# Performance work log

Measured on AMD Instinct MI355X. Metric: run time of the kernel, lower is better.

Reference implementation:

```python
import jax, jax.numpy as jnp
import numpy as np

# Mamba2 config fixed by the wrapper: state=32, expand=1, n_groups=1, conv kernel=4
H, P, N, K = 32, 64, 32, 4          # heads, head_dim, state_size, conv kernel
D_MODEL = H * P                      # hidden = intermediate (expand=1) = 2048
CONV_DIM = D_MODEL + 2 * N           # intermediate + 2*n_groups*state = 2112
PROJ = D_MODEL + CONV_DIM + H        # in_proj width = 4192
EPS = 1e-6


def setup_inputs() -> dict:
    key = jax.random.key(0)
    ks = jax.random.split(key, 8)
    B, L = 4, 2048
    w = lambda k, shape, sc=0.02: jax.random.normal(k, shape, jnp.float32) * sc
    return {
        "x": jax.random.normal(ks[0], (B, L, D_MODEL), jnp.float32),
        "W_in": w(ks[1], (D_MODEL, PROJ)),
        "b_in": jnp.zeros((PROJ,), jnp.float32),
        "conv_w": w(ks[2], (CONV_DIM, K), 0.25),
        "conv_b": jnp.zeros((CONV_DIM,), jnp.float32),
        "A_log": jnp.log(jnp.arange(1, H + 1, dtype=jnp.float32)),
        "dt_bias": jax.random.uniform(ks[3], (H,), jnp.float32, -4.0, 0.0),
        "D_param": jnp.ones((H,), jnp.float32),
        "norm_w": jnp.ones((D_MODEL,), jnp.float32),
        "W_out": w(ks[4], (D_MODEL, D_MODEL)),
    }


def reference(x, W_in, b_in, conv_w, conv_b, A_log, dt_bias, D_param, norm_w, W_out):
    B, L, _ = x.shape
    proj = x @ W_in + b_in                                   # (B,L,PROJ)
    gate, hBC, dt_raw = jnp.split(proj, [D_MODEL, D_MODEL + CONV_DIM], axis=-1)

    # causal depthwise conv1d over time (kernel K, left pad K-1), then SiLU
    hp = jnp.pad(hBC, ((0, 0), (K - 1, 0), (0, 0)))
    conv = conv_b + sum(hp[:, k:k + L, :] * conv_w[:, k] for k in range(K))
    conv = jax.nn.silu(conv)

    xs, Bm, Cm = jnp.split(conv, [D_MODEL, D_MODEL + N], axis=-1)
    xs = xs.reshape(B, L, H, P)                              # (B,L,H,P)

    A = -jnp.exp(A_log)                                      # (H,)
    dt = jax.nn.softplus(dt_raw + dt_bias)                   # (B,L,H)
    dA = jnp.exp(dt * A)                                     # (B,L,H)

    def step(hstate, inp):
        dA_t, dt_t, x_t, B_t, C_t = inp                      # (B,H),(B,H),(B,H,P),(B,N),(B,N)
        upd = (dt_t[:, :, None] * x_t)[..., None] * B_t[:, None, None, :]
        hstate = dA_t[:, :, None, None] * hstate + upd       # (B,H,P,N)
        y_t = jnp.einsum('bhpn,bn->bhp', hstate, C_t)
        return hstate, y_t

    h0 = jnp.zeros((B, H, P, N), x.dtype)
    scan_in = (dA.transpose(1, 0, 2), dt.transpose(1, 0, 2),
               xs.transpose(1, 0, 2, 3), Bm.transpose(1, 0, 2), Cm.transpose(1, 0, 2))
    _, ys = jax.lax.scan(step, h0, scan_in)                  # ys: (L,B,H,P)

    y = ys.transpose(1, 0, 2, 3) + D_param[None, None, :, None] * xs
    y = y.reshape(B, L, D_MODEL)

    # gated RMSNorm: gate applied before normalization (MambaRMSNormGated)
    y = y * jax.nn.silu(gate)
    var = jnp.mean(jnp.square(y), axis=-1, keepdims=True)
    y = y * jax.lax.rsqrt(var + EPS) * norm_w
    return y @ W_out
```

## Files before the change

kernel.cpp:

```cpp
#include <hip/hip_runtime.h>
#include <cstdint>
#include <cstddef>

constexpr int kB    = 4;
constexpr int kL    = 2048;
constexpr int kH    = 32;
constexpr int kP    = 64;
constexpr int kN    = 32;
constexpr int kD    = 2048;
constexpr int kProjW = 4192;
constexpr int kLdp  = 4224;
constexpr int kM    = kB * kL;
constexpr int kK    = kD;
constexpr int kLC   = 64;
constexpr int kNC   = kL / kLC;

typedef _Float16 f16x8 __attribute__((ext_vector_type(8)));
typedef float f32x4 __attribute__((ext_vector_type(4)));

__device__ __forceinline__ float lane_bcast(float v, int lane) {
    return __int_as_float(__builtin_amdgcn_readlane(__float_as_int(v), lane));
}
__device__ __forceinline__ float silu_f(float x) { return x / (1.f + __expf(-x)); }

__device__ __forceinline__ void async_copy16(const void* g, void* lds) {
    __builtin_amdgcn_global_load_lds(
        (const __attribute__((address_space(1))) unsigned int*)(uintptr_t)g,
        (__attribute__((address_space(3))) unsigned int*)(uintptr_t)lds,
        16, 0, 0);
}

__global__ __launch_bounds__(256) void cast_f16_kernel(const float* __restrict__ in,
                                                       _Float16* __restrict__ out) {
    size_t i = ((size_t)blockIdx.x * 256 + threadIdx.x) * 8;
    float4 a = *(const float4*)(in + i);
    float4 b = *(const float4*)(in + i + 4);
    f16x8 o;
    o[0] = (_Float16)a.x; o[1] = (_Float16)a.y; o[2] = (_Float16)a.z; o[3] = (_Float16)a.w;
    o[4] = (_Float16)b.x; o[5] = (_Float16)b.y; o[6] = (_Float16)b.z; o[7] = (_Float16)b.w;
    *(f16x8*)(out + i) = o;
}

__global__ __launch_bounds__(256) void transpose_cast_kernel(const float* __restrict__ W,
                                                             _Float16* __restrict__ Wt,
                                                             int R, int C) {
    __shared__ float tile[32][33];
    const int c0 = blockIdx.x * 32;
    const int r0 = blockIdx.y * 32;
    const int tx = threadIdx.x & 31;
    const int ty = threadIdx.x >> 5;
    #pragma unroll
    for (int i = 0; i < 32; i += 8) {
        int rr = r0 + ty + i;
        int cc = c0 + tx;
        tile[ty + i][tx] = (cc < C) ? W[(size_t)rr * C + cc] : 0.f;
    }
    __syncthreads();
    #pragma unroll
    for (int i = 0; i < 32; i += 8) {
        int cc = c0 + ty + i;
        int rr = r0 + tx;
        Wt[(size_t)cc * R + rr] = (_Float16)tile[tx][ty + i];
    }
}

template <bool OUT_F16>
__global__ __launch_bounds__(256, 2) void gemm128_kernel(
    const _Float16* __restrict__ A, const _Float16* __restrict__ Bt,
    const float* __restrict__ bias,
    void* __restrict__ Cout, int K, int ldc, int nn)
{
    __shared__ __attribute__((aligned(16))) _Float16 lds[3 * 12288];

    const int tid = threadIdx.x;
    const int l = tid & 63, r = l & 15, q = l >> 4;
    const int w = tid >> 6, wm = w >> 1, wn = w & 1;

    const int nwg = gridDim.x;
    const int q8 = nwg >> 3;
    const int pid = blockIdx.x;
    const int wg = (pid & 7) * q8 + (pid >> 3);
    const int m_idx = wg / nn;
    const int n_idx = wg - m_idx * nn;
    const size_t tileM = (size_t)m_idx * 128;
    const size_t tileN = (size_t)n_idx * 256;

    const int sR = ((tid >> 6) << 4) | (tid & 15);
    const int sC = ((tid >> 4) & 3) << 3;
    const _Float16* aSrc = A  + (tileM + sR) * (size_t)K + sC;
    const _Float16* bSrc = Bt + (tileN + sR) * (size_t)K + sC;
    _Float16* dst0 = lds + tid * 8;

    auto STAGE = [&](int buf, int kt2) {
        const _Float16* a = aSrc + kt2 * 32;
        const _Float16* b = bSrc + kt2 * 32;
        _Float16* d = dst0 + buf * 12288;
        async_copy16(a, d);
        async_copy16(a + (size_t)64 * K, d + 2048);
        #pragma unroll
        for (int c = 0; c < 4; ++c)
            async_copy16(b + (size_t)(c * 64) * K, d + 4096 + c * 2048);
    };

    const int NT = K >> 5;
    STAGE(0, 0); STAGE(1, 1);
    asm volatile("s_waitcnt vmcnt(6)" ::: "memory");
    asm volatile("s_barrier" ::: "memory");

    f32x4 acc[4][8] = {};
    f16x8 af[4], bf[8];

    const int aRd = wm * 4096 + l * 16;
    const int bRd = 8192 + wn * 8192 + l * 16;

    int cs = 0;
    for (int kt = 0; kt < NT; ++kt) {
        const char* base = (const char*)lds + cs * 24576;
        if (kt + 2 < NT) {
            int ns = cs + 2; if (ns >= 3) ns -= 3;
            STAGE(ns, kt + 2);
        }
        #pragma unroll
        for (int i = 0; i < 4; ++i)
            af[i] = *(const f16x8*)(base + aRd + i * 1024);
        #pragma unroll
        for (int j = 0; j < 8; ++j)
            bf[j] = *(const f16x8*)(base + bRd + j * 1024);
        asm volatile("s_waitcnt lgkmcnt(0)" ::: "memory");
        __builtin_amdgcn_sched_barrier(0);
        __builtin_amdgcn_s_setprio(1);
        #pragma unroll
        for (int i = 0; i < 4; ++i)
            #pragma unroll
            for (int j = 0; j < 8; ++j)
                acc[i][j] = __builtin_amdgcn_mfma_f32_16x16x32_f16(af[i], bf[j], acc[i][j], 0, 0, 0);
        __builtin_amdgcn_s_setprio(0);
        if (kt + 2 < NT) asm volatile("s_waitcnt vmcnt(6)" ::: "memory");
        else             asm volatile("s_waitcnt vmcnt(0)" ::: "memory");
        asm volatile("s_barrier" ::: "memory");
        cs = (cs + 1 >= 3) ? 0 : cs + 1;
    }

    #pragma unroll
    for (int j = 0; j < 8; ++j) {
        const int col = (int)tileN + wn * 128 + j * 16 + r;
        float bv = 0.f;
        if (bias != nullptr) bv = bias[col];
        #pragma unroll
        for (int i = 0; i < 4; ++i) {
            const size_t row = tileM + (size_t)(wm * 64 + i * 16 + q * 4);
            #pragma unroll
            for (int u = 0; u < 4; ++u) {
                float v = acc[i][j][u] + bv;
                if (OUT_F16) ((_Float16*)Cout)[(row + u) * (size_t)ldc + col] = (_Float16)v;
                else         ((float*)Cout)[(row + u) * (size_t)ldc + col] = v;
            }
        }
    }
}

__global__ __launch_bounds__(256) void gemm_tail_kernel(
    const _Float16* __restrict__ A, const _Float16* __restrict__ Bt,
    const float* __restrict__ bias , _Float16* __restrict__ Cout,
    const float* __restrict__ A_log, const float* __restrict__ dt_bias,
    float* __restrict__ dtv, float* __restrict__ dAv)
{
    __shared__ __attribute__((aligned(16))) _Float16 lds[2 * 10240];
    const int K = kK;
    const int tid = threadIdx.x;
    const int l = tid & 63, r = l & 15, q = l >> 4;
    const int w = tid >> 6;
    const size_t tileM = (size_t)blockIdx.x * 32;

    const int sRa = ((tid >> 7) << 4) | (tid & 15);
    const int sC  = ((tid >> 4) & 7) << 3;
    const _Float16* aSrc = A + (tileM + sRa) * (size_t)K + sC;
    const _Float16* bSrc = Bt + (size_t)sRa * K + sC;
    _Float16* dst0 = lds + tid * 8;

    auto STG = [&](int buf, int kt2) {
        const _Float16* a = aSrc + kt2 * 64;
        const _Float16* b = bSrc + kt2 * 64;
        _Float16* d = dst0 + buf * 10240;
        async_copy16(a, d);
        #pragma unroll
        for (int c = 0; c < 4; ++c)
            async_copy16(b + (size_t)(c * 32) * K, d + 2048 + c * 2048);
    };

    const int NT = K / 64;
    STG(0, 0); STG(1, 1);
    asm volatile("s_waitcnt vmcnt(5)" ::: "memory");
    asm volatile("s_barrier" ::: "memory");

    f32x4 acc[2][2] = {};
    f16x8 af[2][2], bf[2][2];
    const int aRdT = l * 16;
    const int bRdT = 4096 + w * 2 * 2048 + l * 16;

    for (int kt = 0; kt < NT; ++kt) {
        const char* base = (const char*)lds + (kt & 1) * 20480;
        af[0][0] = *(const f16x8*)(base + aRdT);
        af[1][0] = *(const f16x8*)(base + aRdT + 2048);
        af[0][1] = *(const f16x8*)(base + aRdT + 1024);
        af[1][1] = *(const f16x8*)(base + aRdT + 3072);
        bf[0][0] = *(const f16x8*)(base + bRdT);
        bf[1][0] = *(const f16x8*)(base + bRdT + 2048);
        bf[0][1] = *(const f16x8*)(base + bRdT + 1024);
        bf[1][1] = *(const f16x8*)(base + bRdT + 3072);
        asm volatile("s_waitcnt lgkmcnt(0)" ::: "memory");
        __builtin_amdgcn_sched_barrier(0);
        asm volatile("s_barrier" ::: "memory");
        if (kt + 2 < NT) STG(kt & 1, kt + 2);
        #pragma unroll
        for (int kk = 0; kk < 2; ++kk)
            #pragma unroll
            for (int i = 0; i < 2; ++i)
                #pragma unroll
                for (int j = 0; j < 2; ++j)
                    acc[i][j] = __builtin_amdgcn_mfma_f32_16x16x32_f16(af[i][kk], bf[j][kk], acc[i][j], 0, 0, 0);
        if (kt + 2 < NT) asm volatile("s_waitcnt vmcnt(5)" ::: "memory");
        else             asm volatile("s_waitcnt vmcnt(0)" ::: "memory");
        asm volatile("s_barrier" ::: "memory");
    }

    #pragma unroll
    for (int j = 0; j < 2; ++j) {
        const int colOff = w * 32 + j * 16 + r;
        const float bv = (colOff < 96) ? bias[colOff] : 0.f;
        #pragma unroll
        for (int i = 0; i < 2; ++i) {
            #pragma unroll
            for (int u = 0; u < 4; ++u) {
                const size_t row = tileM + (size_t)(i * 16 + q * 4 + u);
                float v = acc[i][j][u] + bv;
                Cout[row * kLdp + 4096 + colOff] = (_Float16)v;
            }
        }
        if (colOff >= 64 && colOff < 96) {
            const int h = colOff - 64;
            const float db = dt_bias[h];
            const float nA = -expf(A_log[h]);
            #pragma unroll
            for (int i = 0; i < 2; ++i) {
                #pragma unroll
                for (int u = 0; u < 4; ++u) {
                    const size_t row = tileM + (size_t)(i * 16 + q * 4 + u);
                    const int b = (int)(row >> 11), t = (int)(row & 2047);
                    float z = acc[i][j][u] + bv + db;
                    float dt = (z > 20.f) ? z : log1pf(expf(z));
                    float dA = expf(dt * nA);
                    const size_t idx = (((size_t)b * kH + h) << 11) | t;
                    dtv[idx] = dt;
                    dAv[idx] = dA;
                }
            }
        }
    }
}

__global__ __launch_bounds__(64) void scan_pass1_kernel(
    const _Float16* __restrict__ projh, const float* __restrict__ conv_w,
    const float* __restrict__ conv_b, const float* __restrict__ dtv,
    const float* __restrict__ dAv, float* __restrict__ cstate, float* __restrict__ Pch)
{
    const int blk = blockIdx.x;
    const int c   = blk & (kNC - 1);
    const int bh  = blk >> 5;
    const int h   = bh & (kH - 1);
    const int b   = bh >> 5;
    const int l   = threadIdx.x;
    const int t0  = c * kLC;

    const int chx = h * kP + l;
    const int chb = 2048 + (l & 31);
    const float xw0 = conv_w[chx*4+0], xw1 = conv_w[chx*4+1], xw2 = conv_w[chx*4+2], xw3 = conv_w[chx*4+3];
    const float xbb = conv_b[chx];
    const float bw0 = conv_w[chb*4+0], bw1 = conv_w[chb*4+1], bw2 = conv_w[chb*4+2], bw3 = conv_w[chb*4+3];
    const float bbb = conv_b[chb];

    const _Float16* pb = projh + (size_t)b * kL * kLdp;
    const int colx = 2048 + chx;
    const int colb = 2048 + chb;

    float xq0=0.f, xq1=0.f, xq2=0.f, bq0=0.f, bq1=0.f, bq2=0.f;
    if (c > 0) {
        xq0 = (float)pb[(size_t)(t0-3)*kLdp + colx];
        xq1 = (float)pb[(size_t)(t0-2)*kLdp + colx];
        xq2 = (float)pb[(size_t)(t0-1)*kLdp + colx];
        bq0 = (float)pb[(size_t)(t0-3)*kLdp + colb];
        bq1 = (float)pb[(size_t)(t0-2)*kLdp + colb];
        bq2 = (float)pb[(size_t)(t0-1)*kLdp + colb];
    }

    float hs[kN];
    #pragma unroll
    for (int n = 0; n < kN; ++n) hs[n] = 0.f;
    float Pp = 1.f;
    const float* dtp = dtv + (size_t)bh * kL;
    const float* dAp = dAv + (size_t)bh * kL;

    float xv = (float)pb[(size_t)t0 * kLdp + colx];
    float bv = (float)pb[(size_t)t0 * kLdp + colb];
    float dt = dtp[t0], dA = dAp[t0];

    #pragma unroll 1
    for (int t = t0; t < t0 + kLC; ++t) {
        float xn = 0.f, bn = 0.f, dtn = 0.f, dAn = 0.f;
        if (t + 1 < t0 + kLC) {
            const size_t ro2 = (size_t)(t + 1) * kLdp;
            xn = (float)pb[ro2 + colx];
            bn = (float)pb[ro2 + colb];
            dtn = dtp[t + 1]; dAn = dAp[t + 1];
        }
        float sx = silu_f(xbb + xw0*xq0 + xw1*xq1 + xw2*xq2 + xw3*xv);
        float sb = silu_f(bbb + bw0*bq0 + bw1*bq1 + bw2*bq2 + bw3*bv);
        xq0=xq1; xq1=xq2; xq2=xv;
        bq0=bq1; bq1=bq2; bq2=bv;
        float dtx = dt * sx;
        Pp *= dA;
        #pragma unroll
        for (int n = 0; n < kN; ++n)
            hs[n] = fmaf(dA, hs[n], dtx * lane_bcast(sb, n));
        xv = xn; bv = bn; dt = dtn; dA = dAn;
    }
    float* cs = cstate + (size_t)blk * (kP * kN) + l * kN;
    #pragma unroll
    for (int n = 0; n < kN; ++n) cs[n] = hs[n];
    if (l == 0) Pch[blk] = Pp;
}

__global__ __launch_bounds__(256) void scan_pass2_kernel(float* __restrict__ cstate,
                                                         const float* __restrict__ Pch) {
    const int bh  = blockIdx.x;
    const int off = threadIdx.x * 8;
    float s[8];
    #pragma unroll
    for (int i = 0; i < 8; ++i) s[i] = 0.f;
    float* base = cstate + (size_t)bh * (kNC * kP * kN) + off;
    #pragma unroll 1
    for (int c = 0; c < kNC; ++c) {
        float* cs = base + c * (kP * kN);
        float Pp = Pch[bh * kNC + c];
        #pragma unroll
        for (int i = 0; i < 8; ++i) {
            float loc = cs[i];
            cs[i] = s[i];
            s[i] = fmaf(Pp, s[i], loc);
        }
    }
}

__global__ __launch_bounds__(64) void scan_pass3_kernel(
    const _Float16* __restrict__ projh, const float* __restrict__ conv_w,
    const float* __restrict__ conv_b, const float* __restrict__ dtv,
    const float* __restrict__ dAv, const float* __restrict__ cstate,
    const float* __restrict__ D_param, float* __restrict__ ypre)
{
    const int blk = blockIdx.x;
    const int c   = blk & (kNC - 1);
    const int bh  = blk >> 5;
    const int h   = bh & (kH - 1);
    const int b   = bh >> 5;
    const int l   = threadIdx.x;
    const int t0  = c * kLC;

    const int chx = h * kP + l;
    const int chc = 2048 + l;
    const float xw0 = conv_w[chx*4+0], xw1 = conv_w[chx*4+1], xw2 = conv_w[chx*4+2], xw3 = conv_w[chx*4+3];
    const float xbb = conv_b[chx];
    const float cw0 = conv_w[chc*4+0], cw1 = conv_w[chc*4+1], cw2 = conv_w[chc*4+2], cw3 = conv_w[chc*4+3];
    const float cbb = conv_b[chc];

    const _Float16* pb = projh + (size_t)b * kL * kLdp;
    const int colx = 2048 + chx;
    const int colc = 2048 + chc;

    float xq0=0.f, xq1=0.f, xq2=0.f, cq0=0.f, cq1=0.f, cq2=0.f;
    if (c > 0) {
        xq0 = (float)pb[(size_t)(t0-3)*kLdp + colx];
        xq1 = (float)pb[(size_t)(t0-2)*kLdp + colx];
        xq2 = (float)pb[(size_t)(t0-1)*kLdp + colx];
        cq0 = (float)pb[(size_t)(t0-3)*kLdp + colc];
        cq1 = (float)pb[(size_t)(t0-2)*kLdp + colc];
        cq2 = (float)pb[(size_t)(t0-1)*kLdp + colc];
    }

    float hs[kN];
    const float* cs = cstate + (size_t)blk * (kP * kN) + l * kN;
    #pragma unroll
    for (int n = 0; n < kN; ++n) hs[n] = cs[n];
    const float Dh = D_param[h];
    const float* dtp = dtv + (size_t)bh * kL;
    const float* dAp = dAv + (size_t)bh * kL;
    float* yo = ypre + (size_t)b * kL * kD + h * kP + l;

    float xv = (float)pb[(size_t)t0 * kLdp + colx];
    float cv = (float)pb[(size_t)t0 * kLdp + colc];
    float dt = dtp[t0], dA = dAp[t0];

    #pragma unroll 1
    for (int t = t0; t < t0 + kLC; ++t) {
        float xn = 0.f, cn2 = 0.f, dtn = 0.f, dAn = 0.f;
        if (t + 1 < t0 + kLC) {
            const size_t ro2 = (size_t)(t + 1) * kLdp;
            xn = (float)pb[ro2 + colx];
            cn2 = (float)pb[ro2 + colc];
            dtn = dtp[t + 1]; dAn = dAp[t + 1];
        }
        float sx = silu_f(xbb + xw0*xq0 + xw1*xq1 + xw2*xq2 + xw3*xv);
        float sc = silu_f(cbb + cw0*cq0 + cw1*cq1 + cw2*cq2 + cw3*cv);
        xq0=xq1; xq1=xq2; xq2=xv;
        cq0=cq1; cq1=cq2; cq2=cv;
        float dtx = dt * sx;
        float y0 = Dh * sx, y1 = 0.f;
        #pragma unroll
        for (int n = 0; n < kN; ++n) {
            float bn = lane_bcast(sc, n);
            float cn = lane_bcast(sc, n + 32);
            hs[n] = fmaf(dA, hs[n], dtx * bn);
            if (n & 1) y1 = fmaf(hs[n], cn, y1);
            else       y0 = fmaf(hs[n], cn, y0);
        }
        yo[(size_t)t * kD] = y0 + y1;
        xv = xn; cv = cn2; dt = dtn; dA = dAn;
    }
}

__global__ __launch_bounds__(256) void gated_norm_kernel(
    const float* __restrict__ ypre, const _Float16* __restrict__ projh,
    const float* __restrict__ norm_w, _Float16* __restrict__ yh)
{
    const int row = blockIdx.x;
    const int tid = threadIdx.x;
    const float* yr = ypre + (size_t)row * kD;
    const _Float16* gr = projh + (size_t)row * kLdp;
    float v[8];
    float ss = 0.f;
    #pragma unroll
    for (int u = 0; u < 8; ++u) {
        int col = tid + u * 256;
        float g = (float)gr[col];
        float t = yr[col] * (g / (1.f + __expf(-g)));
        v[u] = t;
        ss = fmaf(t, t, ss);
    }
    #pragma unroll
    for (int off = 32; off > 0; off >>= 1) ss += __shfl_xor(ss, off, 64);
    __shared__ float red[4];
    if ((tid & 63) == 0) red[tid >> 6] = ss;
    __syncthreads();
    float tot = (red[0] + red[1]) + (red[2] + red[3]);
    float scl = rsqrtf(tot * (1.f / (float)kD) + 1e-6f);
    #pragma unroll
    for (int u = 0; u < 8; ++u) {
        int col = tid + u * 256;
        yh[(size_t)row * kD + col] = (_Float16)(v[u] * scl * norm_w[col]);
    }
}

extern "C" void kernel_launch(void* const* d_in, const int* in_sizes, int n_in,
                              void* d_out, int out_size, void* d_ws, size_t ws_size,
                              hipStream_t stream)
{
    (void)in_sizes; (void)n_in; (void)out_size; (void)ws_size;
    const float* x       = (const float*)d_in[0];
    const float* W_in    = (const float*)d_in[1];
    const float* b_in    = (const float*)d_in[2];
    const float* conv_w  = (const float*)d_in[3];
    const float* conv_b  = (const float*)d_in[4];
    const float* A_log   = (const float*)d_in[5];
    const float* dt_bias = (const float*)d_in[6];
    const float* D_param = (const float*)d_in[7];
    const float* norm_w  = (const float*)d_in[8];
    const float* W_out   = (const float*)d_in[9];
    float* out = (float*)d_out;

    char* p = (char*)d_ws;
    _Float16* projh = (_Float16*)p; p += (size_t)kM * kLdp * 2;
    _Float16* xh    = (_Float16*)p; p += (size_t)kM * kD * 2;
    _Float16* Wt    = (_Float16*)p; p += (size_t)kLdp * kK * 2;
    _Float16* Wot   = (_Float16*)p; p += (size_t)kD * kK * 2;
    float* dtv      = (float*)p;    p += (size_t)kB * kH * kL * 4;
    float* dAv      = (float*)p;    p += (size_t)kB * kH * kL * 4;
    float* Pch      = (float*)p;    p += (size_t)kB * kH * kNC * 4;
    float* cstate = (float*)xh;
    _Float16* yh  = xh;
    float* ypre = out;

    cast_f16_kernel<<<(kM * kD) / (256 * 8), 256, 0, stream>>>(x, xh);
    transpose_cast_kernel<<<dim3(kLdp / 32, kK / 32), 256, 0, stream>>>(W_in, Wt, kK, kProjW);
    transpose_cast_kernel<<<dim3(kD / 32, kK / 32), 256, 0, stream>>>(W_out, Wot, kK, kD);
    gemm128_kernel<true><<<1024, 256, 0, stream>>>(
        xh, Wt, b_in, (void*)projh, kK, kLdp, 16);
    gemm_tail_kernel<<<kM / 32, 256, 0, stream>>>(
        xh, Wt + (size_t)4096 * kK, b_in + 4096, projh, A_log, dt_bias, dtv, dAv);
    scan_pass1_kernel<<<kB * kH * kNC, 64, 0, stream>>>(projh, conv_w, conv_b, dtv, dAv, cstate, Pch);
    scan_pass2_kernel<<<kB * kH, 256, 0, stream>>>(cstate, Pch);
    scan_pass3_kernel<<<kB * kH * kNC, 64, 0, stream>>>(projh, conv_w, conv_b, dtv, dAv, cstate, D_param, ypre);
    gated_norm_kernel<<<kM, 256, 0, stream>>>(ypre, projh, norm_w, yh);
    gemm128_kernel<false><<<512, 256, 0, stream>>>(
        yh, Wot, nullptr, (void*)out, kK, kD, 8);
}
```

Before: 694.3 us.

## Enlarge GEMM tiles to 256x256 with 8 waves and software-pipelined LDS fragment loads

```diff
diff --git a/kernel.cpp b/kernel.cpp
--- a/kernel.cpp
+++ b/kernel.cpp
@@ -11,7 +11,7 @@
 constexpr int kProjW = 4192;
 constexpr int kLdp  = 4224;
 constexpr int kM    = kB * kL;
-constexpr int kK    = kD;
+constexpr int kK    = 2048;
 constexpr int kLC   = 64;
 constexpr int kNC   = kL / kLC;
 
@@ -65,16 +65,16 @@
 }
 
 template <bool OUT_F16>
-__global__ __launch_bounds__(256, 2) void gemm128_kernel(
+__global__ __launch_bounds__(512, 2) void gemm256_kernel(
     const _Float16* __restrict__ A, const _Float16* __restrict__ Bt,
     const float* __restrict__ bias,
-    void* __restrict__ Cout, int K, int ldc, int nn)
+    void* __restrict__ Cout, int ldc, int nn)
 {
-    __shared__ __attribute__((aligned(16))) _Float16 lds[3 * 12288];
+    __shared__ __attribute__((aligned(16))) _Float16 lds[3 * 16384];
 
     const int tid = threadIdx.x;
     const int l = tid & 63, r = l & 15, q = l >> 4;
-    const int w = tid >> 6, wm = w >> 1, wn = w & 1;
+    const int w = tid >> 6, wm = w >> 2, wn = w & 3;
 
     const int nwg = gridDim.x;
     const int q8 = nwg >> 3;
@@ -82,73 +82,100 @@
     const int wg = (pid & 7) * q8 + (pid >> 3);
     const int m_idx = wg / nn;
     const int n_idx = wg - m_idx * nn;
-    const size_t tileM = (size_t)m_idx * 128;
+    const size_t tileM = (size_t)m_idx * 256;
     const size_t tileN = (size_t)n_idx * 256;
 
-    const int sR = ((tid >> 6) << 4) | (tid & 15);
-    const int sC = ((tid >> 4) & 3) << 3;
-    const _Float16* aSrc = A  + (tileM + sR) * (size_t)K + sC;
-    const _Float16* bSrc = Bt + (tileN + sR) * (size_t)K + sC;
+    const int sRow = ((tid >> 6) << 4) + (tid & 15);
+    const int sCol = ((tid >> 4) & 3) << 3;
+    const _Float16* aSrc = A  + (tileM + sRow) * (size_t)kK + sCol;
+    const _Float16* bSrc = Bt + (tileN + sRow) * (size_t)kK + sCol;
     _Float16* dst0 = lds + tid * 8;
 
     auto STAGE = [&](int buf, int kt2) {
         const _Float16* a = aSrc + kt2 * 32;
         const _Float16* b = bSrc + kt2 * 32;
-        _Float16* d = dst0 + buf * 12288;
+        _Float16* d = dst0 + buf * 16384;
         async_copy16(a, d);
-        async_copy16(a + (size_t)64 * K, d + 2048);
-        #pragma unroll
-        for (int c = 0; c < 4; ++c)
-            async_copy16(b + (size_t)(c * 64) * K, d + 4096 + c * 2048);
+        async_copy16(a + (size_t)128 * kK, d + 4096);
+        async_copy16(b, d + 8192);
+        async_copy16(b + (size_t)128 * kK, d + 12288);
     };
 
-    const int NT = K >> 5;
+    constexpr int NT = kK / 32;
+    const char* ldsb = (const char*)lds;
+    const int aRd = wm * 8192 + l * 16;
+    const int bRd = wn * 4096 + l * 16;
+
+    f32x4 acc[8][4] = {};
+    f16x8 af03[4], af47A[4], af47B[4], bfA[4], bfB[4];
+
+#define MFMA_HALF(AFR, BFR, AO)                                                \
+    _Pragma("unroll")                                                          \
+    for (int i = 0; i < 4; ++i)                                                \
+        _Pragma("unroll")                                                      \
+        for (int j = 0; j < 4; ++j)                                            \
+            acc[(AO) + i][j] = __builtin_amdgcn_mfma_f32_16x16x32_f16(         \
+                AFR[i], BFR[j], acc[(AO) + i][j], 0, 0, 0);
+
+#define TILE_BODY(KT, AF47_R, BF_R, AF47_P, BF_P, VM)                          \
+    {                                                                          \
+        asm volatile("s_waitcnt vmcnt(" #VM ")" ::: "memory");                 \
+        asm volatile("s_barrier" ::: "memory");                                \
+        const char* _bp = ldsb + ((KT) % 3) * 32768;                           \
+        _Pragma("unroll")                                                      \
+        for (int i = 0; i < 4; ++i)                                            \
+            af03[i] = *(const f16x8*)(_bp + aRd + i * 1024);                   \
+        _Pragma("unroll")                                                      \
+        for (int i = 0; i < 4; ++i)                                            \
+            AF47_R[i] = *(const f16x8*)(_bp + aRd + (4 + i) * 1024);           \
+        _Pragma("unroll")                                                      \
+        for (int j = 0; j < 4; ++j)                                            \
+            BF_R[j] = *(const f16x8*)(_bp + 16384 + bRd + j * 1024);           \
+        if ((KT) + 2 < NT) STAGE(((KT) + 2) % 3, (KT) + 2);                    \
+        __builtin_amdgcn_sched_barrier(0);                                     \
+        __builtin_amdgcn_s_setprio(1);                                         \
+        MFMA_HALF(AF47_P, BF_P, 4)                                             \
+        asm volatile("s_waitcnt lgkmcnt(0)" ::: "memory");                     \
+        __builtin_amdgcn_sched_barrier(0);                                     \
+        MFMA_HALF(af03, BF_R, 0)                                               \
+        __builtin_amdgcn_s_setprio(0);                                         \
+    }
+
     STAGE(0, 0); STAGE(1, 1);
-    asm volatile("s_waitcnt vmcnt(6)" ::: "memory");
+    asm volatile("s_waitcnt vmcnt(4)" ::: "memory");
     asm volatile("s_barrier" ::: "memory");
-
-    f32x4 acc[4][8] = {};
-    f16x8 af[4], bf[8];
-
-    const int aRd = wm * 4096 + l * 16;
-    const int bRd = 8192 + wn * 8192 + l * 16;
-
-    int cs = 0;
-    for (int kt = 0; kt < NT; ++kt) {
-        const char* base = (const char*)lds + cs * 24576;
-        if (kt + 2 < NT) {
-            int ns = cs + 2; if (ns >= 3) ns -= 3;
-            STAGE(ns, kt + 2);
-        }
-        #pragma unroll
-        for (int i = 0; i < 4; ++i)
-            af[i] = *(const f16x8*)(base + aRd + i * 1024);
-        #pragma unroll
-        for (int j = 0; j < 8; ++j)
-            bf[j] = *(const f16x8*)(base + bRd + j * 1024);
-        asm volatile("s_waitcnt lgkmcnt(0)" ::: "memory");
-        __builtin_amdgcn_sched_barrier(0);
-        __builtin_amdgcn_s_setprio(1);
-        #pragma unroll
-        for (int i = 0; i < 4; ++i)
-            #pragma unroll
-            for (int j = 0; j < 8; ++j)
-                acc[i][j] = __builtin_amdgcn_mfma_f32_16x16x32_f16(af[i], bf[j], acc[i][j], 0, 0, 0);
-        __builtin_amdgcn_s_setprio(0);
-        if (kt + 2 < NT) asm volatile("s_waitcnt vmcnt(6)" ::: "memory");
-        else             asm volatile("s_waitcnt vmcnt(0)" ::: "memory");
-        asm volatile("s_barrier" ::: "memory");
-        cs = (cs + 1 >= 3) ? 0 : cs + 1;
-    }
-
-    #pragma unroll
-    for (int j = 0; j < 8; ++j) {
-        const int col = (int)tileN + wn * 128 + j * 16 + r;
+    #pragma unroll
+    for (int i = 0; i < 4; ++i) af03[i]  = *(const f16x8*)(ldsb + aRd + i * 1024);
+    #pragma unroll
+    for (int i = 0; i < 4; ++i) af47A[i] = *(const f16x8*)(ldsb + aRd + (4 + i) * 1024);
+    #pragma unroll
+    for (int j = 0; j < 4; ++j) bfA[j]   = *(const f16x8*)(ldsb + 16384 + bRd + j * 1024);
+    STAGE(2, 2);
+    asm volatile("s_waitcnt lgkmcnt(0)" ::: "memory");
+    __builtin_amdgcn_sched_barrier(0);
+    __builtin_amdgcn_s_setprio(1);
+    MFMA_HALF(af03, bfA, 0)
+    __builtin_amdgcn_s_setprio(0);
+
+    for (int kt = 1; kt < NT - 1; kt += 2) {
+        TILE_BODY(kt,     af47B, bfB, af47A, bfA, 4)
+        TILE_BODY(kt + 1, af47A, bfA, af47B, bfB, 4)
+    }
+    TILE_BODY(NT - 1, af47B, bfB, af47A, bfA, 0)
+    __builtin_amdgcn_s_setprio(1);
+    MFMA_HALF(af47B, bfB, 4)
+    __builtin_amdgcn_s_setprio(0);
+#undef MFMA_HALF
+#undef TILE_BODY
+
+    #pragma unroll
+    for (int j = 0; j < 4; ++j) {
+        const int col = (int)tileN + wn * 64 + j * 16 + r;
         float bv = 0.f;
         if (bias != nullptr) bv = bias[col];
         #pragma unroll
-        for (int i = 0; i < 4; ++i) {
-            const size_t row = tileM + (size_t)(wm * 64 + i * 16 + q * 4);
+        for (int i = 0; i < 8; ++i) {
+            const size_t row = tileM + (size_t)(wm * 128 + i * 16 + q * 4);
             #pragma unroll
             for (int u = 0; u < 4; ++u) {
                 float v = acc[i][j][u] + bv;
@@ -433,15 +460,19 @@
 {
     const int row = blockIdx.x;
     const int tid = threadIdx.x;
+    const int c0 = tid * 8;
     const float* yr = ypre + (size_t)row * kD;
     const _Float16* gr = projh + (size_t)row * kLdp;
+    float4 ya = *(const float4*)(yr + c0);
+    float4 yb = *(const float4*)(yr + c0 + 4);
+    f16x8 g8 = *(const f16x8*)(gr + c0);
     float v[8];
+    const float yv[8] = {ya.x, ya.y, ya.z, ya.w, yb.x, yb.y, yb.z, yb.w};
     float ss = 0.f;
     #pragma unroll
     for (int u = 0; u < 8; ++u) {
-        int col = tid + u * 256;
-        float g = (float)gr[col];
-        float t = yr[col] * (g / (1.f + __expf(-g)));
+        float g = (float)g8[u];
+        float t = yv[u] * (g / (1.f + __expf(-g)));
         v[u] = t;
         ss = fmaf(t, t, ss);
     }
@@ -452,11 +483,13 @@
     __syncthreads();
     float tot = (red[0] + red[1]) + (red[2] + red[3]);
     float scl = rsqrtf(tot * (1.f / (float)kD) + 1e-6f);
-    #pragma unroll
-    for (int u = 0; u < 8; ++u) {
-        int col = tid + u * 256;
-        yh[(size_t)row * kD + col] = (_Float16)(v[u] * scl * norm_w[col]);
-    }
+    float4 wa = *(const float4*)(norm_w + c0);
+    float4 wb = *(const float4*)(norm_w + c0 + 4);
+    const float wv[8] = {wa.x, wa.y, wa.z, wa.w, wb.x, wb.y, wb.z, wb.w};
+    f16x8 o;
+    #pragma unroll
+    for (int u = 0; u < 8; ++u) o[u] = (_Float16)(v[u] * scl * wv[u]);
+    *(f16x8*)(yh + (size_t)row * kD + c0) = o;
 }
 
 extern "C" void kernel_launch(void* const* d_in, const int* in_sizes, int n_in,
@@ -491,14 +524,14 @@
     cast_f16_kernel<<<(kM * kD) / (256 * 8), 256, 0, stream>>>(x, xh);
     transpose_cast_kernel<<<dim3(kLdp / 32, kK / 32), 256, 0, stream>>>(W_in, Wt, kK, kProjW);
     transpose_cast_kernel<<<dim3(kD / 32, kK / 32), 256, 0, stream>>>(W_out, Wot, kK, kD);
-    gemm128_kernel<true><<<1024, 256, 0, stream>>>(
-        xh, Wt, b_in, (void*)projh, kK, kLdp, 16);
+    gemm256_kernel<true><<<512, 512, 0, stream>>>(
+        xh, Wt, b_in, (void*)projh, kLdp, 16);
     gemm_tail_kernel<<<kM / 32, 256, 0, stream>>>(
         xh, Wt + (size_t)4096 * kK, b_in + 4096, projh, A_log, dt_bias, dtv, dAv);
     scan_pass1_kernel<<<kB * kH * kNC, 64, 0, stream>>>(projh, conv_w, conv_b, dtv, dAv, cstate, Pch);
     scan_pass2_kernel<<<kB * kH, 256, 0, stream>>>(cstate, Pch);
     scan_pass3_kernel<<<kB * kH * kNC, 64, 0, stream>>>(projh, conv_w, conv_b, dtv, dAv, cstate, D_param, ypre);
     gated_norm_kernel<<<kM, 256, 0, stream>>>(ypre, projh, norm_w, yh);
-    gemm128_kernel<false><<<512, 256, 0, stream>>>(
-        yh, Wot, nullptr, (void*)out, kK, kD, 8);
-}
+    gemm256_kernel<false><<<256, 512, 0, stream>>>(
+        yh, Wot, nullptr, (void*)out, kD, 8);
+}
```

Result: faster. 651.0 us (-6.2%).
